# Kernel optimization log

Hardware: AMD Instinct MI355X
Metric: run time of the kernel (lower is better)

The kernel has to match this reference:

```python
import jax, jax.numpy as jnp
import numpy as np

B, N, C = 2, 2048, 2048
H, KV = 16, 4          # query heads, kv heads
D = C // H             # head_dim = 128
ROPE_BASE = 10000.0


def rope_cos_sin(position_ids, dim):
    # interleaved RoPE: freqs for even indices, repeated pairwise to full dim
    inv_freq = 1.0 / (ROPE_BASE ** (jnp.arange(0, dim, 2, dtype=jnp.float32) / dim))
    ang = position_ids[..., None].astype(jnp.float32) * inv_freq   # [B, N, D/2]
    cos = jnp.repeat(jnp.cos(ang), 2, axis=-1)                     # [B, N, D]
    sin = jnp.repeat(jnp.sin(ang), 2, axis=-1)
    return cos, sin


def rotate_half_interleaved(x):
    # (x0, x1, x2, x3, ...) -> (-x1, x0, -x3, x2, ...)
    x1 = x[..., 0::2]
    x2 = x[..., 1::2]
    return jnp.stack([-x2, x1], axis=-1).reshape(x.shape)


def apply_rotary(x, cos, sin):
    # x: [B, h, N, D]; cos/sin: [B, N, D]
    return x * cos[:, None] + rotate_half_interleaved(x) * sin[:, None]


def setup_inputs() -> dict:
    key = jax.random.key(0)
    ks = jax.random.split(key, 5)
    s = 0.02
    return dict(
        x=jax.random.normal(ks[0], (B, N, C), jnp.float32),
        position_ids=jnp.tile(jnp.arange(N, dtype=jnp.int32), (B, 1)),
        Wq=jax.random.normal(ks[1], (C, C), jnp.float32) * s,
        bq=jnp.zeros((C,), jnp.float32),
        Wk=jax.random.normal(ks[2], (C, KV * D), jnp.float32) * s,
        bk=jnp.zeros((KV * D,), jnp.float32),
        Wv=jax.random.normal(ks[3], (C, KV * D), jnp.float32) * s,
        bv=jnp.zeros((KV * D,), jnp.float32),
        Wo=jax.random.normal(ks[4], (C, C), jnp.float32) * s,
    )


def reference(x, position_ids, Wq, bq, Wk, bk, Wv, bv, Wo):
    Bx, Nx, Cx = x.shape
    q = (x @ Wq + bq).reshape(Bx, Nx, H, D).transpose(0, 2, 1, 3)   # [B,H,N,D]
    k = (x @ Wk + bk).reshape(Bx, Nx, KV, D).transpose(0, 2, 1, 3)  # [B,KV,N,D]
    v = (x @ Wv + bv).reshape(Bx, Nx, KV, D).transpose(0, 2, 1, 3)

    cos, sin = rope_cos_sin(position_ids, D)
    q = apply_rotary(q, cos, sin)
    k = apply_rotary(k, cos, sin)

    # GQA expand: head h uses kv head h // groups (matches unsqueeze+expand+reshape)
    groups = H // KV
    k = jnp.repeat(k, groups, axis=1)   # [B,H,N,D]
    v = jnp.repeat(v, groups, axis=1)

    attn = jnp.einsum('bhqd,bhkd->bhqk', q, k) * (D ** -0.5)        # [B,H,N,N]
    causal_mask = jnp.triu(jnp.ones((Nx, Nx), dtype=bool), 1)
    attn = jnp.where(causal_mask, -jnp.inf, attn)
    attn = jax.nn.softmax(attn, axis=-1)

    out = jnp.einsum('bhqk,bhkd->bhqd', attn, v)
    out = out.transpose(0, 2, 1, 3).reshape(Bx, Nx, Cx)
    return out @ Wo
```

## Files before the change

### kernel.cpp

```cpp
#include <hip/hip_runtime.h>
#include <cstdint>
#include <type_traits>

typedef unsigned short u16;
typedef unsigned int u32;
typedef __bf16 bf16x8 __attribute__((ext_vector_type(8)));
typedef float f32x4 __attribute__((ext_vector_type(4)));

constexpr int BB = 2;
constexpr int SEQ = 2048;
constexpr int CH = 2048;
constexpr int NH = 16;
constexpr int NKV = 4;
constexpr int HD = 128;
constexpr int QKVC = CH + 2 * NKV * HD;

#define DI __device__ __forceinline__

DI u16 f2b(float x) {
  u32 u = __float_as_uint(x);
  u = u + 0x7FFFu + ((u >> 16) & 1u);
  return (u16)(u >> 16);
}
DI float b2f(u16 u) { return __uint_as_float(((u32)u) << 16); }

DI u32 pack2bf(float lo, float hi) {
  return __builtin_amdgcn_perm(__float_as_uint(hi), __float_as_uint(lo), 0x07060302u);
}

DI void glds16(const void* g, void* l) {
  __builtin_amdgcn_global_load_lds(
      (__attribute__((address_space(1))) void*)(uintptr_t)g,
      (__attribute__((address_space(3))) void*)(u32)(uintptr_t)l, 16, 0, 0);
}

__global__ __launch_bounds__(256) void xconv_kernel(const float* __restrict__ in,
                                                    u16* __restrict__ out, int n4) {
  int i = blockIdx.x * 256 + threadIdx.x;
  if (i < n4) {
    float4 v = *(const float4*)&in[(size_t)i * 4];
    ushort4 o;
    o.x = f2b(v.x); o.y = f2b(v.y); o.z = f2b(v.z); o.w = f2b(v.w);
    *(ushort4*)&out[(size_t)i * 4] = o;
  }
}

__global__ __launch_bounds__(256) void wtrans4_kernel(
    const float* __restrict__ Wq, const float* __restrict__ Wk,
    const float* __restrict__ Wv, const float* __restrict__ Wo,
    u16* __restrict__ wqkvt, u16* __restrict__ wot) {
  const int z = blockIdx.z;
  const float* in;
  u16* out;
  int Cc;
  if (z == 0)      { in = Wq; out = wqkvt;                                Cc = CH; }
  else if (z == 1) { in = Wk; out = wqkvt + (size_t)CH * CH;              Cc = NKV * HD; }
  else if (z == 2) { in = Wv; out = wqkvt + (size_t)(CH + NKV * HD) * CH; Cc = NKV * HD; }
  else             { in = Wo; out = wot;                                  Cc = CH; }
  if ((int)blockIdx.y * 64 >= Cc) return;

  __shared__ u16 tile[64 * 65];
  const int r0 = blockIdx.x * 64, c0 = blockIdx.y * 64;
  const int tid = threadIdx.x;
  for (int c = tid; c < 1024; c += 256) {
    int r = c >> 4, col = (c & 15) * 4;
    float4 v = *(const float4*)&in[(size_t)(r0 + r) * Cc + c0 + col];
    tile[r * 65 + col + 0] = f2b(v.x);
    tile[r * 65 + col + 1] = f2b(v.y);
    tile[r * 65 + col + 2] = f2b(v.z);
    tile[r * 65 + col + 3] = f2b(v.w);
  }
  __syncthreads();
  for (int c = tid; c < 1024; c += 256) {
    int r = c >> 4, col = (c & 15) * 4;
    ushort4 v;
    v.x = tile[(col + 0) * 65 + r];
    v.y = tile[(col + 1) * 65 + r];
    v.z = tile[(col + 2) * 65 + r];
    v.w = tile[(col + 3) * 65 + r];
    *(ushort4*)&out[(size_t)(c0 + r) * CH + r0 + col] = v;
  }
}

__global__ __launch_bounds__(256) void vtrans_kernel(const u16* __restrict__ in,
                                                     u16* __restrict__ out) {
  __shared__ u16 tile[64 * 65];
  const int s = blockIdx.z, n0 = blockIdx.x * 64, d0 = blockIdx.y * 64;
  const int tid = threadIdx.x;
  const u16* ip = in + (size_t)s * SEQ * HD + (size_t)n0 * HD + d0;
  u16* op = out + (size_t)s * HD * SEQ + (size_t)d0 * SEQ + n0;
  for (int c = tid; c < 1024; c += 256) {
    int r = c >> 4, col = (c & 15) * 4;
    ushort4 v = *(const ushort4*)&ip[(size_t)r * HD + col];
    tile[r * 65 + col + 0] = v.x;
    tile[r * 65 + col + 1] = v.y;
    tile[r * 65 + col + 2] = v.z;
    tile[r * 65 + col + 3] = v.w;
  }
  __syncthreads();
  for (int c = tid; c < 1024; c += 256) {
    int r = c >> 4, col = (c & 15) * 4;
    ushort4 v;
    v.x = tile[(col + 0) * 65 + r];
    v.y = tile[(col + 1) * 65 + r];
    v.z = tile[(col + 2) * 65 + r];
    v.w = tile[(col + 3) * 65 + r];
    int u = col;
    int w = (u & 3) | (((u >> 5) & 1) << 2) | (((u >> 2) & 3) << 3) | (((u >> 4) & 1) << 5);
    int glp = (w >> 3) ^ (r & 7);
    int colp = glp * 8 + (w & 7);
    *(ushort4*)&op[(size_t)r * SEQ + colp] = v;
  }
}

template <int MODE>
__global__ __launch_bounds__(512, 2) void gemm256_kernel(
    const u16* __restrict__ A, const u16* __restrict__ Bt,
    u16* __restrict__ Cb, float* __restrict__ Cf, u16* __restrict__ Vn,
    const float* __restrict__ bq, const float* __restrict__ bk,
    const float* __restrict__ bv, int M, int Nn, int K) {
  constexpr int BM = (MODE == 0) ? 256 : 128;
  constexpr int MI = BM / 32;
  extern __shared__ char smem[];
  u16* As = (u16*)smem;
  u16* Bs = As + 2 * BM * 64;

  const int tid = threadIdx.x;
  const int lane = tid & 63, wave = tid >> 6;
  const int wrow = wave >> 2, wcol = wave & 3;
  const int lm = lane & 15, lq = lane >> 4;
  const int m0 = blockIdx.x * BM, n0 = blockIdx.y * 256;
  const int l8 = lane >> 3;
  const int sswz8 = ((lane & 7) ^ l8) * 8;

  f32x4 acc[MI][4] = {};

  auto stageA = [&](int kt, int bsel, int half) {
    if constexpr (MODE == 0) {
#pragma unroll
      for (int j = 0; j < 2; j++) {
        const int rb = wave * 8 + j * 128 + half * 64;
        glds16(A + (size_t)(m0 + rb + l8) * K + kt + sswz8,
               (char*)As + bsel * (BM * 128) + rb * 128);
      }
    } else {
      const int rb = (wave & 3) * 8 + (wave >> 2) * 64 + half * 32;
      glds16(A + (size_t)(m0 + rb + l8) * K + kt + sswz8,
             (char*)As + bsel * (BM * 128) + rb * 128);
    }
  };
  auto stageB = [&](int kt, int bsel, int half) {
#pragma unroll
    for (int j = 0; j < 2; j++) {
      const int rb = (wave & 3) * 8 + (j * 2 + (wave >> 2)) * 64 + half * 32;
      glds16(Bt + (size_t)(n0 + rb + l8) * K + kt + sswz8,
             (char*)Bs + bsel * 32768 + rb * 128);
    }
  };

  const int NT = K >> 6;
  stageA(0, 0, 0); stageB(0, 0, 0); stageB(0, 0, 1); stageA(0, 0, 1);
  asm volatile("s_waitcnt vmcnt(0)" ::: "memory");
  __builtin_amdgcn_s_barrier();

  if constexpr (MODE == 0) {
    bf16x8 bf[2][2][2];
    for (int T = 0; T < NT; T++) {
      const int buf = T & 1;
      const u16* Asb = As + buf * (BM * 64);
      const u16* Bsb = Bs + buf * (256 * 64);
      const int kt1 = (T + 1) << 6;
      const bool pf = (T + 1 < NT);
      bf16x8 af[4][2];
#pragma unroll
      for (int q = 0; q < 4; q++) {
        const int qm = q >> 1, qn = q & 1;
        if (qn == 0) {
#pragma unroll
          for (int ii = 0; ii < 4; ii++)
#pragma unroll
            for (int kk = 0; kk < 2; kk++)
              af[ii][kk] = *(const bf16x8*)&Asb[(wrow * 128 + qm * 64 + ii * 16 + lm) * 64 +
                                                ((kk * 4 + lq) ^ (lm & 7)) * 8];
        }
        if (q < 2) {
#pragma unroll
          for (int jj = 0; jj < 2; jj++)
#pragma unroll
            for (int kk = 0; kk < 2; kk++)
              bf[qn][jj][kk] = *(const bf16x8*)&Bsb[(wcol * 64 + qn * 32 + jj * 16 + lm) * 64 +
                                                    ((kk * 4 + lq) ^ (lm & 7)) * 8];
        }
        if (pf) {
          if (q == 0) stageA(kt1, buf ^ 1, 0);
          else if (q == 1) stageB(kt1, buf ^ 1, 0);
          else if (q == 2) stageB(kt1, buf ^ 1, 1);
          else stageA(kt1, buf ^ 1, 1);
        }
        __builtin_amdgcn_s_barrier();
        asm volatile("s_waitcnt lgkmcnt(0)" ::: "memory");
        __builtin_amdgcn_sched_barrier(0);
        __builtin_amdgcn_s_setprio(1);
#pragma unroll
        for (int kk = 0; kk < 2; kk++)
#pragma unroll
          for (int ii = 0; ii < 4; ii++)
#pragma unroll
            for (int jj = 0; jj < 2; jj++)
              acc[qm * 4 + ii][qn * 2 + jj] = __builtin_amdgcn_mfma_f32_16x16x32_bf16(
                  af[ii][kk], bf[qn][jj][kk], acc[qm * 4 + ii][qn * 2 + jj], 0, 0, 0);
        __builtin_amdgcn_s_setprio(0);
        if (q == 0) {
          if (pf) asm volatile("s_waitcnt vmcnt(4)" ::: "memory");
          else    asm volatile("s_waitcnt vmcnt(2)" ::: "memory");
        } else if (q == 1) {
          if (pf) asm volatile("s_waitcnt vmcnt(4)" ::: "memory");
          else    asm volatile("s_waitcnt vmcnt(0)" ::: "memory");
        } else if (q == 3 && pf) {
          asm volatile("s_waitcnt vmcnt(4)" ::: "memory");
        }
        __builtin_amdgcn_s_barrier();
      }
    }
  } else {
    bf16x8 bf1[4][2];
    for (int T = 0; T < NT; T++) {
      const int buf = T & 1;
      const u16* Asb = As + buf * (BM * 64);
      const u16* Bsb = Bs + buf * (256 * 64);
      const int kt1 = (T + 1) << 6;
      const bool pf = (T + 1 < NT);
      bf16x8 af[2][2];
#pragma unroll
      for (int q = 0; q < 2; q++) {
#pragma unroll
        for (int ii = 0; ii < 2; ii++)
#pragma unroll
          for (int kk = 0; kk < 2; kk++)
            af[ii][kk] = *(const bf16x8*)&Asb[(wrow * 64 + (q * 2 + ii) * 16 + lm) * 64 +
                                              ((kk * 4 + lq) ^ (lm & 7)) * 8];
        if (q == 0) {
#pragma unroll
          for (int j = 0; j < 4; j++)
#pragma unroll
            for (int kk = 0; kk < 2; kk++)
              bf1[j][kk] = *(const bf16x8*)&Bsb[(wcol * 64 + j * 16 + lm) * 64 +
                                                ((kk * 4 + lq) ^ (lm & 7)) * 8];
        }
        if (pf) {
          if (q == 0) { stageA(kt1, buf ^ 1, 0); stageB(kt1, buf ^ 1, 0); stageB(kt1, buf ^ 1, 1); }
          else stageA(kt1, buf ^ 1, 1);
        }
        __builtin_amdgcn_s_barrier();
        asm volatile("s_waitcnt lgkmcnt(0)" ::: "memory");
        __builtin_amdgcn_sched_barrier(0);
        __builtin_amdgcn_s_setprio(1);
#pragma unroll
        for (int kk = 0; kk < 2; kk++)
#pragma unroll
          for (int ii = 0; ii < 2; ii++)
#pragma unroll
            for (int j = 0; j < 4; j++)
              acc[q * 2 + ii][j] = __builtin_amdgcn_mfma_f32_16x16x32_bf16(
                  af[ii][kk], bf1[j][kk], acc[q * 2 + ii][j], 0, 0, 0);
        __builtin_amdgcn_s_setprio(0);
        if (q == 0) {
          if (pf) asm volatile("s_waitcnt vmcnt(5)" ::: "memory");
          else    asm volatile("s_waitcnt vmcnt(0)" ::: "memory");
        } else if (pf) {
          asm volatile("s_waitcnt vmcnt(1)" ::: "memory");
        }
        __builtin_amdgcn_s_barrier();
      }
    }
  }

#pragma unroll
  for (int i = 0; i < MI; i++) {
    const int mg = m0 + wrow * (BM / 2) + i * 16 + lq * 4;
#pragma unroll
    for (int j = 0; j < 4; j++) {
      const int ng = n0 + wcol * 64 + j * 16 + lm;
      float bias = 0.f;
      if (MODE == 0)
        bias = (ng < CH) ? bq[ng] : (ng < CH + NKV * HD ? bk[ng - CH] : bv[ng - CH - NKV * HD]);
#pragma unroll
      for (int r = 0; r < 4; r++) {
        float v = acc[i][j][r] + bias;
        if (MODE == 0) {
          if (ng >= CH + NKV * HD) {
            int tok = mg + r;
            int bidx = tok >> 11, n = tok & (SEQ - 1);
            int vcol = ng - (CH + NKV * HD);
            int kh = vcol >> 7, d = vcol & (HD - 1);
            Vn[((size_t)(bidx * NKV + kh) * SEQ + n) * HD + d] = f2b(v);
          } else {
            Cb[(size_t)(mg + r) * Nn + ng] = f2b(v);
          }
        } else {
          Cf[(size_t)(mg + r) * Nn + ng] = v;
        }
      }
    }
  }
}

__global__ __launch_bounds__(256) void rope_kernel(
    const u16* __restrict__ qkv, const int* __restrict__ pos,
    u16* __restrict__ Qo, u16* __restrict__ Ko) {
  __shared__ float cs_s[64], sn_s[64];
  const int tok = blockIdx.x;
  const int b = tok >> 11, n = tok & (SEQ - 1);
  const int t = threadIdx.x;
  const u16* row = qkv + (size_t)tok * QKVC;
  const float LN1E4_64 = 0.14391156831212788f;

  if (t < 64) {
    float ang = (float)pos[tok] * expf(-(float)t * LN1E4_64);
    float sn, cs;
    sincosf(ang, &sn, &cs);
    cs_s[t] = cs;
    sn_s[t] = sn;
  }
  __syncthreads();

  for (int idx = t; idx < NH * 64; idx += 256) {
    int hh = idx >> 6, i = idx & 63;
    float cs = cs_s[i], sn = sn_s[i];
    float q0v = b2f(row[hh * 128 + 2 * i]);
    float q1v = b2f(row[hh * 128 + 2 * i + 1]);
    size_t off = ((size_t)(b * NH + hh) * SEQ + n) * HD + 2 * i;
    Qo[off] = f2b(q0v * cs - q1v * sn);
    Qo[off + 1] = f2b(q1v * cs + q0v * sn);
  }
  {
    int kh = t >> 6, i = t & 63;
    float cs = cs_s[i], sn = sn_s[i];
    float k0v = b2f(row[CH + kh * 128 + 2 * i]);
    float k1v = b2f(row[CH + kh * 128 + 2 * i + 1]);
    int d0 = 2 * i;
    int g = d0 >> 3;
    int gp = (g & 8) | ((g ^ n) & 7);
    int dp = gp * 8 + (d0 & 7);
    size_t off = ((size_t)(b * NKV + kh) * SEQ + n) * HD + dp;
    Ko[off] = f2b(k0v * cs - k1v * sn);
    Ko[off + 1] = f2b(k1v * cs + k0v * sn);
  }
}

__global__ __launch_bounds__(256, 2) void flash_kernel(
    const u16* __restrict__ Q, const u16* __restrict__ Kk,
    const u16* __restrict__ Vt, u16* __restrict__ Oo) {
  __shared__ u16 Kb[2][64 * 128];
  __shared__ u16 Vb[2][144 * 64];
  const int tid = threadIdx.x, lane = tid & 63, wave = tid >> 6;
  const int lm = lane & 15, lq = lane >> 4;
  const int p = blockIdx.x;
  const int h = blockIdx.y, b = blockIdx.z;
  const int q0A = p * 64, q0B = (31 - p) * 64;
  const int kvh = h >> 2;
  const u16* Qg = Q + (size_t)(b * NH + h) * SEQ * HD;
  const u16* Kg = Kk + (size_t)(b * NKV + kvh) * SEQ * HD;
  const u16* Vg = Vt + (size_t)(b * NKV + kvh) * HD * SEQ;

  if (tid < 128) Vb[tid >> 6][128 * 64 + (tid & 63)] = 0x3F80;

  bf16x8 qf[2][4];
#pragma unroll
  for (int qg = 0; qg < 2; qg++) {
    const int q0g = qg ? q0B : q0A;
    const u16* qrow = Qg + (size_t)(q0g + wave * 16 + lm) * HD;
#pragma unroll
    for (int kd = 0; kd < 4; kd++)
      qf[qg][kd] = *(const bf16x8*)&qrow[kd * 32 + lq * 8];
  }

  f32x4 oacc[2][8] = {};
  f32x4 oaccS[2] = {};
  const float SCL2 = 0.12754325f;
  const int nIter = 32 - p;

  auto stage = [&](int kv0, int bufi) {
    const char* kb = (const char*)(Kg + (size_t)kv0 * HD);
    char* kl = (char*)&Kb[bufi][0];
    const char* vbb = (const char*)(Vg + (size_t)kv0);
    char* vl = (char*)&Vb[bufi][0];
#pragma unroll
    for (int c = 0; c < 4; c++) {
      int ch = wave * 4 + c;
      glds16(kb + ch * 1024 + lane * 16, kl + ch * 1024);
      glds16(vbb + (size_t)(ch * 8 + (lane >> 3)) * (SEQ * 2) + (lane & 7) * 16,
             vl + ch * 1024);
    }
  };

  stage(0, 0);

  for (int t = 0; t < nIter; t++) {
    __syncthreads();
    if (t + 1 < nIter) stage((t + 1) * 64, (t + 1) & 1);
    const u16* Ks = &Kb[t & 1][0];
    const u16* Vs = &Vb[t & 1][0];
    const int kv0 = t * 64;
    const bool actA = (t <= p);

    auto run = [&](auto dualc) {
      constexpr bool DUAL = decltype(dualc)::value;
      f32x4 sv[2][4] = {};
#pragma unroll
      for (int nt = 0; nt < 4; nt++)
#pragma unroll
        for (int kd = 0; kd < 4; kd++) {
          int g = kd * 4 + lq;
          int gpp = (g & 8) | ((g ^ lm) & 7);
          bf16x8 kf = *(const bf16x8*)&Ks[(nt * 16 + lm) * 128 + gpp * 8];
          sv[1][nt] = __builtin_amdgcn_mfma_f32_16x16x32_bf16(kf, qf[1][kd], sv[1][nt], 0, 0, 0);
          if constexpr (DUAL)
            sv[0][nt] = __builtin_amdgcn_mfma_f32_16x16x32_bf16(kf, qf[0][kd], sv[0][nt], 0, 0, 0);
        }

      alignas(16) u32 pad[2][2][4];
      auto softmax = [&](int qg, int q0g) {
        const int base = q0g + wave * 16;
        if (kv0 + 63 > base) {
          const int qrow = base + lm;
#pragma unroll
          for (int nt = 0; nt < 4; nt++) {
            float pv[4];
#pragma unroll
            for (int r = 0; r < 4; r++) {
              int kvg = kv0 + nt * 16 + lq * 4 + r;
              float e = exp2f(sv[qg][nt][r] * SCL2);
              pv[r] = (kvg > qrow) ? 0.f : e;
            }
            pad[qg][nt & 1][(nt >> 1) * 2 + 0] = pack2bf(pv[0], pv[1]);
            pad[qg][nt & 1][(nt >> 1) * 2 + 1] = pack2bf(pv[2], pv[3]);
          }
        } else {
#pragma unroll
          for (int nt = 0; nt < 4; nt++) {
            float pv[4];
#pragma unroll
            for (int r = 0; r < 4; r++) pv[r] = exp2f(sv[qg][nt][r] * SCL2);
            pad[qg][nt & 1][(nt >> 1) * 2 + 0] = pack2bf(pv[0], pv[1]);
            pad[qg][nt & 1][(nt >> 1) * 2 + 1] = pack2bf(pv[2], pv[3]);
          }
        }
      };
      softmax(1, q0B);
      if constexpr (DUAL) softmax(0, q0A);

#pragma unroll
      for (int ks = 0; ks < 2; ks++) {
        const int glp = (ks * 4 + lq) ^ (lm & 7);
        const bf16x8 pa1 = *(const bf16x8*)&pad[1][ks][0];
        const bf16x8 pa0 = *(const bf16x8*)&pad[0][ks][0];
#pragma unroll
        for (int dt = 0; dt < 8; dt++) {
          bf16x8 vf = *(const bf16x8*)&Vs[(dt * 16 + lm) * 64 + glp * 8];
          oacc[1][dt] = __builtin_amdgcn_mfma_f32_16x16x32_bf16(pa1, vf, oacc[1][dt], 0, 0, 0);
          if constexpr (DUAL)
            oacc[0][dt] = __builtin_amdgcn_mfma_f32_16x16x32_bf16(pa0, vf, oacc[0][dt], 0, 0, 0);
        }
        bf16x8 vf8 = *(const bf16x8*)&Vs[(128 + lm) * 64 + glp * 8];
        oaccS[1] = __builtin_amdgcn_mfma_f32_16x16x32_bf16(pa1, vf8, oaccS[1], 0, 0, 0);
        if constexpr (DUAL)
          oaccS[0] = __builtin_amdgcn_mfma_f32_16x16x32_bf16(pa0, vf8, oaccS[0], 0, 0, 0);
      }
    };
    if (actA) run(std::integral_constant<bool, true>{});
    else      run(std::integral_constant<bool, false>{});
  }

  u16* orow = Oo + (size_t)b * SEQ * CH + (size_t)h * HD;
#pragma unroll
  for (int qg = 0; qg < 2; qg++) {
    const int q0g = qg ? q0B : q0A;
    float inv[4];
#pragma unroll
    for (int r = 0; r < 4; r++) inv[r] = 1.0f / __shfl(oaccS[qg][r], lq * 16);
    const int qrow_base = q0g + wave * 16 + lq * 4;
#pragma unroll
    for (int dt = 0; dt < 8; dt++)
#pragma unroll
      for (int r = 0; r < 4; r++)
        orow[(size_t)(qrow_base + r) * CH + dt * 16 + lm] = f2b(oacc[qg][dt][r] * inv[r]);
  }
}

extern "C" void kernel_launch(void* const* d_in, const int* in_sizes, int n_in,
                              void* d_out, int out_size, void* d_ws, size_t ws_size,
                              hipStream_t stream) {
  const float* x = (const float*)d_in[0];
  const int* pos = (const int*)d_in[1];
  const float* Wq = (const float*)d_in[2];
  const float* bq = (const float*)d_in[3];
  const float* Wk = (const float*)d_in[4];
  const float* bk = (const float*)d_in[5];
  const float* Wv = (const float*)d_in[6];
  const float* bv = (const float*)d_in[7];
  const float* Wo = (const float*)d_in[8];
  float* out = (float*)d_out;

  char* ws = (char*)d_ws;
  u16* xb = (u16*)ws;    ws += (size_t)BB * SEQ * CH * 2;
  u16* wqkvt = (u16*)ws; ws += (size_t)QKVC * CH * 2;
  u16* wot = (u16*)ws;   ws += (size_t)CH * CH * 2;
  u16* qkv = (u16*)ws;   ws += (size_t)BB * SEQ * QKVC * 2;
  u16* qr = (u16*)ws;    ws += (size_t)BB * NH * SEQ * HD * 2;
  u16* kr = (u16*)ws;    ws += (size_t)BB * NKV * SEQ * HD * 2;
  u16* vn = (u16*)ws;    ws += (size_t)BB * NKV * SEQ * HD * 2;
  u16* vt = (u16*)ws;    ws += (size_t)BB * NKV * SEQ * HD * 2;
  u16* ao = (u16*)ws;    ws += (size_t)BB * SEQ * CH * 2;

  static int attr_done = 0;
  if (!attr_done) {
    hipFuncSetAttribute(reinterpret_cast<const void*>(gemm256_kernel<0>),
                        hipFuncAttributeMaxDynamicSharedMemorySize, 131072);
    hipFuncSetAttribute(reinterpret_cast<const void*>(gemm256_kernel<1>),
                        hipFuncAttributeMaxDynamicSharedMemorySize, 131072);
    attr_done = 1;
  }

  xconv_kernel<<<dim3(BB * SEQ * CH / 1024), 256, 0, stream>>>(x, xb, BB * SEQ * CH / 4);
  wtrans4_kernel<<<dim3(32, 32, 4), 256, 0, stream>>>(Wq, Wk, Wv, Wo, wqkvt, wot);
  gemm256_kernel<0><<<dim3(16, 12), 512, 131072, stream>>>(xb, wqkvt, qkv, (float*)nullptr,
                                                           vn, bq, bk, bv, BB * SEQ, QKVC, CH);
  rope_kernel<<<dim3(BB * SEQ), 256, 0, stream>>>(qkv, pos, qr, kr);
  vtrans_kernel<<<dim3(SEQ / 64, HD / 64, BB * NKV), 256, 0, stream>>>(vn, vt);
  flash_kernel<<<dim3(16, NH, BB), 256, 0, stream>>>(qr, kr, vt, ao);
  gemm256_kernel<1><<<dim3(32, 8), 512, 98304, stream>>>(ao, wot, (u16*)nullptr, out, nullptr,
                                                         nullptr, nullptr, nullptr, BB * SEQ, CH, CH);
}
```

Before: 314.1 us.

## Retile QKV GEMM to 128x384 blocks with three-phase B staging

The fused QKV projection GEMM moves from 256x256 tiles on a 16x12 grid to 128x384 tiles on a 32x8 grid. Each wave now owns a 64x96 output patch, and the K loop runs three phases, one per 128-column slice of B. Staging, swizzled addressing and vmcnt waits are rewritten to match. The aim is 256 blocks, which fills the 256 CUs exactly, instead of 192, at the cost of a changed operand reuse ratio and a more intricate B-tile mapping.

```diff
diff --git a/kernel.cpp b/kernel.cpp
--- a/kernel.cpp
+++ b/kernel.cpp
@@ -119,8 +119,9 @@
     u16* __restrict__ Cb, float* __restrict__ Cf, u16* __restrict__ Vn,
     const float* __restrict__ bq, const float* __restrict__ bk,
     const float* __restrict__ bv, int M, int Nn, int K) {
-  constexpr int BM = (MODE == 0) ? 256 : 128;
-  constexpr int MI = BM / 32;
+  constexpr int BM = 128;
+  constexpr int BN = (MODE == 0) ? 384 : 256;
+  constexpr int NJ = (MODE == 0) ? 6 : 4;
   extern __shared__ char smem[];
   u16* As = (u16*)smem;
   u16* Bs = As + 2 * BM * 64;
@@ -129,73 +130,60 @@
   const int lane = tid & 63, wave = tid >> 6;
   const int wrow = wave >> 2, wcol = wave & 3;
   const int lm = lane & 15, lq = lane >> 4;
-  const int m0 = blockIdx.x * BM, n0 = blockIdx.y * 256;
-  const int l8 = lane >> 3;
-  const int sswz8 = ((lane & 7) ^ l8) * 8;
-
-  f32x4 acc[MI][4] = {};
-
-  auto stageA = [&](int kt, int bsel, int half) {
-    if constexpr (MODE == 0) {
-#pragma unroll
-      for (int j = 0; j < 2; j++) {
-        const int rb = wave * 8 + j * 128 + half * 64;
-        glds16(A + (size_t)(m0 + rb + l8) * K + kt + sswz8,
-               (char*)As + bsel * (BM * 128) + rb * 128);
-      }
-    } else {
-      const int rb = (wave & 3) * 8 + (wave >> 2) * 64 + half * 32;
-      glds16(A + (size_t)(m0 + rb + l8) * K + kt + sswz8,
-             (char*)As + bsel * (BM * 128) + rb * 128);
-    }
-  };
-  auto stageB = [&](int kt, int bsel, int half) {
-#pragma unroll
-    for (int j = 0; j < 2; j++) {
-      const int rb = (wave & 3) * 8 + (j * 2 + (wave >> 2)) * 64 + half * 32;
-      glds16(Bt + (size_t)(n0 + rb + l8) * K + kt + sswz8,
-             (char*)Bs + bsel * 32768 + rb * 128);
-    }
-  };
+  const int m0 = blockIdx.x * BM, n0 = blockIdx.y * BN;
+  const int rr = tid >> 3;
+  const int sswz8 = ((tid & 7) ^ (rr & 7)) * 8;
+
+  f32x4 acc[4][NJ] = {};
 
   const int NT = K >> 6;
-  stageA(0, 0, 0); stageB(0, 0, 0); stageB(0, 0, 1); stageA(0, 0, 1);
-  asm volatile("s_waitcnt vmcnt(0)" ::: "memory");
-  __builtin_amdgcn_s_barrier();
 
   if constexpr (MODE == 0) {
-    bf16x8 bf[2][2][2];
+    auto stA = [&](int kt, int bsel, int h) {
+      glds16(A + (size_t)(m0 + h * 64 + rr) * K + kt + sswz8,
+             (char*)As + bsel * (BM * 128) + (h * 64 + wave * 8) * 128);
+    };
+    auto stB = [&](int kt, int bsel, int q, int s) {
+      int g = 96 * ((s * 64 + rr) >> 5) + 32 * q + (rr & 31);
+      glds16(Bt + (size_t)(n0 + g) * K + kt + sswz8,
+             (char*)Bs + bsel * (BN * 128) + (q * 128 + s * 64 + wave * 8) * 128);
+    };
+
+    stA(0, 0, 0); stA(0, 0, 1);
+    stB(0, 0, 0, 0); stB(0, 0, 0, 1);
+    stB(0, 0, 1, 0); stB(0, 0, 1, 1);
+    stB(0, 0, 2, 0); stB(0, 0, 2, 1);
+    asm volatile("s_waitcnt vmcnt(0)" ::: "memory");
+    __builtin_amdgcn_s_barrier();
+
+    bf16x8 af[4][2];
     for (int T = 0; T < NT; T++) {
-      const int buf = T & 1;
+      const int buf = T & 1, nb = buf ^ 1;
       const u16* Asb = As + buf * (BM * 64);
-      const u16* Bsb = Bs + buf * (256 * 64);
+      const u16* Bsb = Bs + buf * (BN * 64);
       const int kt1 = (T + 1) << 6;
       const bool pf = (T + 1 < NT);
-      bf16x8 af[4][2];
-#pragma unroll
-      for (int q = 0; q < 4; q++) {
-        const int qm = q >> 1, qn = q & 1;
-        if (qn == 0) {
+#pragma unroll
+      for (int q = 0; q < 3; q++) {
+        if (q == 0) {
 #pragma unroll
           for (int ii = 0; ii < 4; ii++)
 #pragma unroll
             for (int kk = 0; kk < 2; kk++)
-              af[ii][kk] = *(const bf16x8*)&Asb[(wrow * 128 + qm * 64 + ii * 16 + lm) * 64 +
+              af[ii][kk] = *(const bf16x8*)&Asb[(wrow * 64 + ii * 16 + lm) * 64 +
                                                 ((kk * 4 + lq) ^ (lm & 7)) * 8];
         }
-        if (q < 2) {
-#pragma unroll
-          for (int jj = 0; jj < 2; jj++)
-#pragma unroll
-            for (int kk = 0; kk < 2; kk++)
-              bf[qn][jj][kk] = *(const bf16x8*)&Bsb[(wcol * 64 + qn * 32 + jj * 16 + lm) * 64 +
-                                                    ((kk * 4 + lq) ^ (lm & 7)) * 8];
-        }
+        bf16x8 bfq[2][2];
+#pragma unroll
+        for (int jj = 0; jj < 2; jj++)
+#pragma unroll
+          for (int kk = 0; kk < 2; kk++)
+            bfq[jj][kk] = *(const bf16x8*)&Bsb[(q * 128 + wcol * 32 + jj * 16 + lm) * 64 +
+                                               ((kk * 4 + lq) ^ (lm & 7)) * 8];
         if (pf) {
-          if (q == 0) stageA(kt1, buf ^ 1, 0);
-          else if (q == 1) stageB(kt1, buf ^ 1, 0);
-          else if (q == 2) stageB(kt1, buf ^ 1, 1);
-          else stageA(kt1, buf ^ 1, 1);
+          if (q == 0) { stA(kt1, nb, 0); stA(kt1, nb, 1); stB(kt1, nb, 0, 0); stB(kt1, nb, 0, 1); }
+          else if (q == 1) { stB(kt1, nb, 1, 0); stB(kt1, nb, 1, 1); }
+          else { stB(kt1, nb, 2, 0); stB(kt1, nb, 2, 1); }
         }
         __builtin_amdgcn_s_barrier();
         asm volatile("s_waitcnt lgkmcnt(0)" ::: "memory");
@@ -207,22 +195,40 @@
           for (int ii = 0; ii < 4; ii++)
 #pragma unroll
             for (int jj = 0; jj < 2; jj++)
-              acc[qm * 4 + ii][qn * 2 + jj] = __builtin_amdgcn_mfma_f32_16x16x32_bf16(
-                  af[ii][kk], bf[qn][jj][kk], acc[qm * 4 + ii][qn * 2 + jj], 0, 0, 0);
+              acc[ii][q * 2 + jj] = __builtin_amdgcn_mfma_f32_16x16x32_bf16(
+                  af[ii][kk], bfq[jj][kk], acc[ii][q * 2 + jj], 0, 0, 0);
         __builtin_amdgcn_s_setprio(0);
         if (q == 0) {
-          if (pf) asm volatile("s_waitcnt vmcnt(4)" ::: "memory");
+          if (pf) asm volatile("s_waitcnt vmcnt(6)" ::: "memory");
           else    asm volatile("s_waitcnt vmcnt(2)" ::: "memory");
         } else if (q == 1) {
-          if (pf) asm volatile("s_waitcnt vmcnt(4)" ::: "memory");
+          if (pf) asm volatile("s_waitcnt vmcnt(6)" ::: "memory");
           else    asm volatile("s_waitcnt vmcnt(0)" ::: "memory");
-        } else if (q == 3 && pf) {
+        } else if (pf) {
           asm volatile("s_waitcnt vmcnt(4)" ::: "memory");
         }
         __builtin_amdgcn_s_barrier();
       }
     }
   } else {
+    auto stageA = [&](int kt, int bsel, int half) {
+      const int rb = (wave & 3) * 8 + (wave >> 2) * 64 + half * 32;
+      glds16(A + (size_t)(m0 + rb + (lane >> 3)) * K + kt + sswz8,
+             (char*)As + bsel * (BM * 128) + rb * 128);
+    };
+    auto stageB = [&](int kt, int bsel, int half) {
+#pragma unroll
+      for (int j = 0; j < 2; j++) {
+        const int rb = (wave & 3) * 8 + (j * 2 + (wave >> 2)) * 64 + half * 32;
+        glds16(Bt + (size_t)(n0 + rb + (lane >> 3)) * K + kt + sswz8,
+               (char*)Bs + bsel * 32768 + rb * 128);
+      }
+    };
+
+    stageA(0, 0, 0); stageB(0, 0, 0); stageB(0, 0, 1); stageA(0, 0, 1);
+    asm volatile("s_waitcnt vmcnt(0)" ::: "memory");
+    __builtin_amdgcn_s_barrier();
+
     bf16x8 bf1[4][2];
     for (int T = 0; T < NT; T++) {
       const int buf = T & 1;
@@ -276,11 +282,11 @@
   }
 
 #pragma unroll
-  for (int i = 0; i < MI; i++) {
-    const int mg = m0 + wrow * (BM / 2) + i * 16 + lq * 4;
-#pragma unroll
-    for (int j = 0; j < 4; j++) {
-      const int ng = n0 + wcol * 64 + j * 16 + lm;
+  for (int i = 0; i < 4; i++) {
+    const int mg = m0 + wrow * 64 + i * 16 + lq * 4;
+#pragma unroll
+    for (int j = 0; j < NJ; j++) {
+      const int ng = n0 + wcol * (NJ * 16) + j * 16 + lm;
       float bias = 0.f;
       if (MODE == 0)
         bias = (ng < CH) ? bq[ng] : (ng < CH + NKV * HD ? bk[ng - CH] : bv[ng - CH - NKV * HD]);
@@ -524,8 +530,8 @@
 
   xconv_kernel<<<dim3(BB * SEQ * CH / 1024), 256, 0, stream>>>(x, xb, BB * SEQ * CH / 4);
   wtrans4_kernel<<<dim3(32, 32, 4), 256, 0, stream>>>(Wq, Wk, Wv, Wo, wqkvt, wot);
-  gemm256_kernel<0><<<dim3(16, 12), 512, 131072, stream>>>(xb, wqkvt, qkv, (float*)nullptr,
-                                                           vn, bq, bk, bv, BB * SEQ, QKVC, CH);
+  gemm256_kernel<0><<<dim3(32, 8), 512, 131072, stream>>>(xb, wqkvt, qkv, (float*)nullptr,
+                                                          vn, bq, bk, bv, BB * SEQ, QKVC, CH);
   rope_kernel<<<dim3(BB * SEQ), 256, 0, stream>>>(qkv, pos, qr, kr);
   vtrans_kernel<<<dim3(SEQ / 64, HD / 64, BB * NKV), 256, 0, stream>>>(vn, vt);
   flash_kernel<<<dim3(16, NH, BB), 256, 0, stream>>>(qr, kr, vt, ao);
```

Result: faster. 300.2 us (-4.4%).
